# Kernel tuning notes

Measured on AMD Instinct MI355X. Metric: run time of the kernel, lower is better.

The kernel has to match this reference:

```python
import jax, jax.numpy as jnp
import numpy as np

C_Z, H, C = 128, 4, 32
L = 320
SCALE = 1.0 / np.sqrt(C)
EPS = 1e-5


def setup_inputs() -> dict:
    key = jax.random.key(0)
    ks = jax.random.split(key, 8)
    s = 0.02
    return {
        "z": jax.random.normal(ks[0], (L, L, C_Z), dtype=jnp.float32),
        "pair_mask": jnp.ones((L, L), dtype=jnp.float32),
        "res_mask": jnp.ones((L,), dtype=bool),
        "ln_gamma": jnp.ones((C_Z,), dtype=jnp.float32),
        "ln_beta": jnp.zeros((C_Z,), dtype=jnp.float32),
        "Wq": jax.random.normal(ks[1], (C_Z, H * C), dtype=jnp.float32) * s,
        "Wk": jax.random.normal(ks[2], (C_Z, H * C), dtype=jnp.float32) * s,
        "Wv": jax.random.normal(ks[3], (C_Z, H * C), dtype=jnp.float32) * s,
        "Wb": jax.random.normal(ks[4], (C_Z, H), dtype=jnp.float32) * s,
        "Wg": jax.random.normal(ks[5], (C_Z, H * C), dtype=jnp.float32) * s,
        "Wout": jax.random.normal(ks[6], (H * C, C_Z), dtype=jnp.float32) * s,
    }


def _layernorm(x, gamma, beta):
    mu = jnp.mean(x, axis=-1, keepdims=True)
    var = jnp.mean(jnp.square(x - mu), axis=-1, keepdims=True)
    return (x - mu) * jax.lax.rsqrt(var + EPS) * gamma + beta


def reference(z, pair_mask, res_mask, ln_gamma, ln_beta, Wq, Wk, Wv, Wb, Wg, Wout):
    Ldim = z.shape[0]
    z_ln = _layernorm(z, ln_gamma, ln_beta)                      # [L,L,c_z]
    Q = (z_ln @ Wq).reshape(Ldim, Ldim, H, C)                    # [i,j,h,c]
    K = (z_ln @ Wk).reshape(Ldim, Ldim, H, C)                    # [i,k,h,c]
    V = (z_ln @ Wv).reshape(Ldim, Ldim, H, C)                    # [i,k,h,c]
    B = z_ln @ Wb                                                # [j,k,h]
    G = jax.nn.sigmoid(z_ln @ Wg).reshape(Ldim, Ldim, H, C)      # [i,j,h,c]

    # logits[i,h,j,k] = <Q[i,j], K[i,k]> * scale + B[j,k,h]
    logits = jnp.einsum("ijhc,ikhc->ihjk", Q, K) * SCALE
    logits = logits + jnp.transpose(B, (2, 0, 1))[None]          # +[1,h,j,k]
    neg_inf = jnp.asarray(-jnp.inf, logits.dtype)
    logits = jnp.where(res_mask[None, None, None, :], logits, neg_inf)
    attn = jax.nn.softmax(logits, axis=-1)                       # over k

    out = jnp.einsum("ihjk,ikhc->ijhc", attn, V)                 # [i,j,h,c]
    out = (G * out).reshape(Ldim, Ldim, H * C)
    dz = out @ Wout                                              # [L,L,c_z]
    return dz * pair_mask[..., None]
```

## Files before the change

kernel.cpp:

```cpp
#include <hip/hip_runtime.h>

#define LDIM 320
#define CZ 128
#define NH 4
#define CH 32
#define SCALE_QK 0.17677669529663687f
#define LN_EPS 1e-5f

typedef __attribute__((ext_vector_type(8))) short bf16x8;
typedef __attribute__((ext_vector_type(4))) float f32x4;

__device__ __forceinline__ unsigned int pack_bf2(float a, float b) {
  unsigned int ua = __float_as_uint(a);
  unsigned int ub = __float_as_uint(b);
  unsigned int ra = (ua + 0x7fffu + ((ua >> 16) & 1u)) >> 16;
  unsigned int rb = (ub + 0x7fffu + ((ub >> 16) & 1u)) >> 16;
  return (ra & 0xffffu) | (rb << 16);
}

__device__ __forceinline__ unsigned short f2bf(float a) {
  unsigned int ua = __float_as_uint(a);
  return (unsigned short)((ua + 0x7fffu + ((ua >> 16) & 1u)) >> 16);
}

__device__ __forceinline__ float bf2f(unsigned short u) {
  return __uint_as_float(((unsigned int)u) << 16);
}

__global__ __launch_bounds__(256) void k_prep(
    const float* __restrict__ Wq, const float* __restrict__ Wk,
    const float* __restrict__ Wv, const float* __restrict__ Wb,
    const float* __restrict__ Wg, const float* __restrict__ Wout,
    unsigned short* __restrict__ Wt, unsigned short* __restrict__ Woutt)
{
  __shared__ __attribute__((aligned(16))) unsigned short buf[64 * 136];
  const int t = threadIdx.x, bid = blockIdx.x;
  const bool isOut = (bid >= 9);
  const int n0 = isOut ? (bid - 9) * 64 : bid * 64;
  const int nl = t & 63;
  const int n = n0 + nl;
#pragma unroll 8
  for (int it = 0; it < 32; ++it) {
    const int k = (t >> 6) + 4 * it;
    float v;
    if (isOut)        v = Wout[k * 128 + n];
    else if (n < 128) v = Wq[k * 128 + n];
    else if (n < 256) v = Wk[k * 128 + n - 128];
    else if (n < 384) v = Wv[k * 128 + n - 256];
    else if (n < 512) v = Wg[k * 128 + n - 384];
    else if (n < 516) v = Wb[k * 4 + n - 512];
    else              v = 0.f;
    buf[nl * 136 + k] = f2bf(v);
  }
  __syncthreads();
  unsigned short* dst = isOut ? Woutt : Wt;
#pragma unroll
  for (int it = 0; it < 4; ++it) {
    const int idx = t + 256 * it;
    const int rr = idx >> 4, ck = idx & 15;
    const uint4 d = *(const uint4*)&buf[rr * 136 + ck * 8];
    *(uint4*)(dst + (size_t)(n0 + rr) * 128 + ck * 8) = d;
  }
}

__global__ __launch_bounds__(256) void k_lnproj(
    const float* __restrict__ z, const float* __restrict__ gamma,
    const float* __restrict__ beta, const unsigned short* __restrict__ Wt,
    unsigned short* __restrict__ Qg, unsigned short* __restrict__ Kg,
    unsigned short* __restrict__ Vg, unsigned short* __restrict__ Gg,
    float* __restrict__ Bh)
{
  __shared__ __attribute__((aligned(16))) unsigned short As[128 * 136];
  const int t = threadIdx.x;
  const int m0 = blockIdx.x * 128;
  const int rlane = t & 7;

  const float* gp = gamma + rlane * 16;
  const float* bp = beta + rlane * 16;
  const float4 g0 = *(const float4*)(gp + 0);
  const float4 g1 = *(const float4*)(gp + 4);
  const float4 g2 = *(const float4*)(gp + 8);
  const float4 g3 = *(const float4*)(gp + 12);
  const float4 b0 = *(const float4*)(bp + 0);
  const float4 b1 = *(const float4*)(bp + 4);
  const float4 b2 = *(const float4*)(bp + 8);
  const float4 b3 = *(const float4*)(bp + 12);

#pragma unroll
  for (int rr = 0; rr < 4; ++rr) {
    const int row = rr * 32 + (t >> 3);
    const float* zp = z + (size_t)(m0 + row) * CZ + rlane * 16;
    const float4 x0 = *(const float4*)(zp + 0);
    const float4 x1 = *(const float4*)(zp + 4);
    const float4 x2 = *(const float4*)(zp + 8);
    const float4 x3 = *(const float4*)(zp + 12);
    float s  = x0.x + x0.y + x0.z + x0.w + x1.x + x1.y + x1.z + x1.w +
               x2.x + x2.y + x2.z + x2.w + x3.x + x3.y + x3.z + x3.w;
    float ss = x0.x*x0.x + x0.y*x0.y + x0.z*x0.z + x0.w*x0.w +
               x1.x*x1.x + x1.y*x1.y + x1.z*x1.z + x1.w*x1.w +
               x2.x*x2.x + x2.y*x2.y + x2.z*x2.z + x2.w*x2.w +
               x3.x*x3.x + x3.y*x3.y + x3.z*x3.z + x3.w*x3.w;
    s  += __shfl_xor(s, 1);  ss += __shfl_xor(ss, 1);
    s  += __shfl_xor(s, 2);  ss += __shfl_xor(ss, 2);
    s  += __shfl_xor(s, 4);  ss += __shfl_xor(ss, 4);
    const float mu  = s * (1.f / 128.f);
    const float var = ss * (1.f / 128.f) - mu * mu;
    const float rs  = rsqrtf(var + LN_EPS);
    uint4 u0, u1;
    u0.x = pack_bf2((x0.x - mu) * rs * g0.x + b0.x, (x0.y - mu) * rs * g0.y + b0.y);
    u0.y = pack_bf2((x0.z - mu) * rs * g0.z + b0.z, (x0.w - mu) * rs * g0.w + b0.w);
    u0.z = pack_bf2((x1.x - mu) * rs * g1.x + b1.x, (x1.y - mu) * rs * g1.y + b1.y);
    u0.w = pack_bf2((x1.z - mu) * rs * g1.z + b1.z, (x1.w - mu) * rs * g1.w + b1.w);
    u1.x = pack_bf2((x2.x - mu) * rs * g2.x + b2.x, (x2.y - mu) * rs * g2.y + b2.y);
    u1.y = pack_bf2((x2.z - mu) * rs * g2.z + b2.z, (x2.w - mu) * rs * g2.w + b2.w);
    u1.z = pack_bf2((x3.x - mu) * rs * g3.x + b3.x, (x3.y - mu) * rs * g3.y + b3.y);
    u1.w = pack_bf2((x3.z - mu) * rs * g3.z + b3.z, (x3.w - mu) * rs * g3.w + b3.w);
    unsigned short* dst = &As[row * 136 + rlane * 16];
    *(uint4*)(dst + 0) = u0;
    *(uint4*)(dst + 8) = u1;
  }
  __syncthreads();

  const int w = t >> 6, lane = t & 63;
  const int m16 = lane & 15, qd = lane >> 4;
  const f32x4 z4 = {0.f, 0.f, 0.f, 0.f};

  bf16x8 af[2][4];
#pragma unroll
  for (int ks = 0; ks < 4; ++ks) {
    af[0][ks] = *(const bf16x8*)&As[(w * 32 + m16) * 136 + ks * 32 + qd * 8];
    af[1][ks] = *(const bf16x8*)&As[(w * 32 + 16 + m16) * 136 + ks * 32 + qd * 8];
  }

  for (int ntile = 0; ntile < 8; ++ntile) {
    f32x4 acc[2][4];
#pragma unroll
    for (int sub = 0; sub < 2; ++sub)
#pragma unroll
      for (int nt = 0; nt < 4; ++nt) acc[sub][nt] = z4;
#pragma unroll
    for (int ks = 0; ks < 4; ++ks) {
#pragma unroll
      for (int nt = 0; nt < 4; ++nt) {
        const bf16x8 bf = *(const bf16x8*)(
            Wt + (size_t)(ntile * 64 + nt * 16 + m16) * 128 + ks * 32 + qd * 8);
        acc[0][nt] = __builtin_amdgcn_mfma_f32_16x16x32_bf16(af[0][ks], bf, acc[0][nt], 0, 0, 0);
        acc[1][nt] = __builtin_amdgcn_mfma_f32_16x16x32_bf16(af[1][ks], bf, acc[1][nt], 0, 0, 0);
      }
    }
#pragma unroll
    for (int sub = 0; sub < 2; ++sub) {
#pragma unroll
      for (int r = 0; r < 4; ++r) {
        const int p = m0 + w * 32 + sub * 16 + qd * 4 + r;
        const int a = p / 320, bb = p - a * 320;
#pragma unroll
        for (int nt = 0; nt < 4; ++nt) {
          const int n = ntile * 64 + nt * 16 + m16;
          const int off = n & 127, hh = off >> 5, cc = off & 31;
          float val = acc[sub][nt][r];
          if (ntile >= 6) val = 1.f / (1.f + __expf(-val));
          unsigned short* dst =
              (ntile < 2 ? Qg : (ntile < 4 ? Kg : (ntile < 6 ? Vg : Gg)));
          dst[((size_t)(a * 4 + hh) * 320 + bb) * 32 + cc] = f2bf(val);
        }
      }
    }
  }

  {
    f32x4 acc0 = z4, acc1 = z4;
#pragma unroll
    for (int ks = 0; ks < 4; ++ks) {
      const bf16x8 bf = *(const bf16x8*)(
          Wt + (size_t)(512 + m16) * 128 + ks * 32 + qd * 8);
      acc0 = __builtin_amdgcn_mfma_f32_16x16x32_bf16(af[0][ks], bf, acc0, 0, 0, 0);
      acc1 = __builtin_amdgcn_mfma_f32_16x16x32_bf16(af[1][ks], bf, acc1, 0, 0, 0);
    }
    if (m16 < 4) {
#pragma unroll
      for (int r = 0; r < 4; ++r) {
        const int p0 = m0 + w * 32 + qd * 4 + r;
        Bh[(size_t)m16 * 102400 + p0] = acc0[r];
        Bh[(size_t)m16 * 102400 + p0 + 16] = acc1[r];
      }
    }
  }
}

__global__ __launch_bounds__(256) void k_attn(
    const unsigned short* __restrict__ Qg, const unsigned short* __restrict__ Kg,
    const unsigned short* __restrict__ Vg, const unsigned short* __restrict__ Gg,
    const float* __restrict__ Bh, const int* __restrict__ rmask,
    unsigned short* __restrict__ Obg)
{
  __shared__ __attribute__((aligned(16))) unsigned short Vt[32 * 328];
  __shared__ __attribute__((aligned(16))) unsigned short Ps[4][16 * 168];
  const int h = blockIdx.x, i = blockIdx.y;
  const int t = threadIdx.x;
  const size_t base = (size_t)(i * NH + h) * (LDIM * CH);

  {
    const int k0 = t >> 3, c4 = (t & 7) * 4;
#pragma unroll
    for (int it = 0; it < 10; ++it) {
      const int k = k0 + 32 * it;
      const uint2 d = *(const uint2*)(Vg + base + k * 32 + c4);
      Vt[(c4 + 0) * 328 + k] = (unsigned short)(d.x & 0xffffu);
      Vt[(c4 + 1) * 328 + k] = (unsigned short)(d.x >> 16);
      Vt[(c4 + 2) * 328 + k] = (unsigned short)(d.y & 0xffffu);
      Vt[(c4 + 3) * 328 + k] = (unsigned short)(d.y >> 16);
    }
  }
  __syncthreads();

  const int w = t >> 6, lane = t & 63;
  const int m16 = lane & 15, qd = lane >> 4;
  const f32x4 z4 = {0.f, 0.f, 0.f, 0.f};

  float mkr[20];
#pragma unroll
  for (int kt = 0; kt < 20; ++kt)
    mkr[kt] = rmask[kt * 16 + m16] ? 0.f : -INFINITY;

  for (int jt = w; jt < 20; jt += 4) {
    const bf16x8 qfrag =
        *(const bf16x8*)(Qg + base + (size_t)(jt * 16 + m16) * 32 + qd * 8);

    f32x4 acc[20];
#pragma unroll
    for (int kt = 0; kt < 20; ++kt) {
      const bf16x8 kf =
          *(const bf16x8*)(Kg + base + (size_t)(kt * 16 + m16) * 32 + qd * 8);
      acc[kt] = __builtin_amdgcn_mfma_f32_16x16x32_bf16(qfrag, kf, z4, 0, 0, 0);
    }

    const float* bp = Bh + (size_t)h * 102400 +
                      (size_t)(jt * 16 + qd * 4) * 320 + m16;
    float mx[4] = {-INFINITY, -INFINITY, -INFINITY, -INFINITY};
#pragma unroll
    for (int kt = 0; kt < 20; ++kt) {
#pragma unroll
      for (int r = 0; r < 4; ++r) {
        const float b = bp[r * 320 + kt * 16];
        const float s = fmaf(acc[kt][r], SCALE_QK, b) + mkr[kt];
        acc[kt][r] = s;
        mx[r] = fmaxf(mx[r], s);
      }
    }
#pragma unroll
    for (int r = 0; r < 4; ++r) {
      mx[r] = fmaxf(mx[r], __shfl_xor(mx[r], 1));
      mx[r] = fmaxf(mx[r], __shfl_xor(mx[r], 2));
      mx[r] = fmaxf(mx[r], __shfl_xor(mx[r], 4));
      mx[r] = fmaxf(mx[r], __shfl_xor(mx[r], 8));
    }
    float l[4] = {0.f, 0.f, 0.f, 0.f};
#pragma unroll
    for (int kt = 0; kt < 20; ++kt) {
#pragma unroll
      for (int r = 0; r < 4; ++r) {
        const float p = __expf(acc[kt][r] - mx[r]);
        acc[kt][r] = p;
        l[r] += p;
      }
    }
#pragma unroll
    for (int r = 0; r < 4; ++r) {
      l[r] += __shfl_xor(l[r], 1);
      l[r] += __shfl_xor(l[r], 2);
      l[r] += __shfl_xor(l[r], 4);
      l[r] += __shfl_xor(l[r], 8);
    }
    float rl[4];
#pragma unroll
    for (int r = 0; r < 4; ++r) rl[r] = 1.f / l[r];

    f32x4 accO0 = z4, accO1 = z4;
#pragma unroll
    for (int hh = 0; hh < 2; ++hh) {
      __syncthreads();
#pragma unroll
      for (int kt2 = 0; kt2 < 10; ++kt2) {
        const int kt = hh * 10 + kt2;
#pragma unroll
        for (int r = 0; r < 4; ++r)
          Ps[w][(qd * 4 + r) * 168 + kt2 * 16 + m16] = f2bf(acc[kt][r] * rl[r]);
      }
      __syncthreads();
#pragma unroll
      for (int ks = 0; ks < 5; ++ks) {
        const bf16x8 pf = *(const bf16x8*)&Ps[w][m16 * 168 + ks * 32 + qd * 8];
        const bf16x8 v0 =
            *(const bf16x8*)&Vt[m16 * 328 + hh * 160 + ks * 32 + qd * 8];
        const bf16x8 v1 =
            *(const bf16x8*)&Vt[(16 + m16) * 328 + hh * 160 + ks * 32 + qd * 8];
        accO0 = __builtin_amdgcn_mfma_f32_16x16x32_bf16(pf, v0, accO0, 0, 0, 0);
        accO1 = __builtin_amdgcn_mfma_f32_16x16x32_bf16(pf, v1, accO1, 0, 0, 0);
      }
    }

#pragma unroll
    for (int r = 0; r < 4; ++r) {
      const int j = jt * 16 + qd * 4 + r;
      const float g0 = bf2f(Gg[base + (size_t)j * 32 + m16]);
      const float g1 = bf2f(Gg[base + (size_t)j * 32 + 16 + m16]);
      unsigned short* op = Obg + (size_t)(i * 320 + j) * 128 + h * 32;
      op[m16]      = f2bf(g0 * accO0[r]);
      op[16 + m16] = f2bf(g1 * accO1[r]);
    }
  }
}

__global__ __launch_bounds__(256) void k_out(
    const unsigned short* __restrict__ Obg, const unsigned short* __restrict__ Woutt,
    const float* __restrict__ pm, float* __restrict__ out)
{
  __shared__ __attribute__((aligned(16))) unsigned short As[128 * 136];
  __shared__ __attribute__((aligned(16))) unsigned short Bs[64 * 136];
  const int t = threadIdx.x;
  const int ntile = blockIdx.x;
  const int m0 = blockIdx.y * 128;

#pragma unroll
  for (int it = 0; it < 8; ++it) {
    const int idx = t + 256 * it;
    const int rr = idx >> 4, ck = idx & 15;
    const uint4 d = *(const uint4*)(Obg + (size_t)(m0 + rr) * 128 + ck * 8);
    *(uint4*)&As[rr * 136 + ck * 8] = d;
  }
  {
    const unsigned short* wrow = Woutt + (size_t)ntile * 64 * 128;
#pragma unroll
    for (int it = 0; it < 4; ++it) {
      const int idx = t + 256 * it;
      const int n = idx >> 4, ck = idx & 15;
      const uint4 d = *(const uint4*)(wrow + n * 128 + ck * 8);
      *(uint4*)&Bs[n * 136 + ck * 8] = d;
    }
  }
  __syncthreads();

  const int w = t >> 6, lane = t & 63;
  const int m16 = lane & 15, qd = lane >> 4;
  const f32x4 z4 = {0.f, 0.f, 0.f, 0.f};
  f32x4 acc[2][4];
#pragma unroll
  for (int sub = 0; sub < 2; ++sub)
#pragma unroll
    for (int nt = 0; nt < 4; ++nt) acc[sub][nt] = z4;

#pragma unroll
  for (int ks = 0; ks < 4; ++ks) {
    const bf16x8 af0 = *(const bf16x8*)&As[(w * 32 + m16) * 136 + qd * 8 + ks * 32];
    const bf16x8 af1 = *(const bf16x8*)&As[(w * 32 + 16 + m16) * 136 + qd * 8 + ks * 32];
#pragma unroll
    for (int nt = 0; nt < 4; ++nt) {
      const bf16x8 bf = *(const bf16x8*)&Bs[(nt * 16 + m16) * 136 + qd * 8 + ks * 32];
      acc[0][nt] = __builtin_amdgcn_mfma_f32_16x16x32_bf16(af0, bf, acc[0][nt], 0, 0, 0);
      acc[1][nt] = __builtin_amdgcn_mfma_f32_16x16x32_bf16(af1, bf, acc[1][nt], 0, 0, 0);
    }
  }

#pragma unroll
  for (int sub = 0; sub < 2; ++sub) {
#pragma unroll
    for (int r = 0; r < 4; ++r) {
      const int p = m0 + w * 32 + sub * 16 + qd * 4 + r;
      const float m = pm[p];
      float* orow = out + (size_t)p * 128 + ntile * 64;
#pragma unroll
      for (int nt = 0; nt < 4; ++nt)
        orow[nt * 16 + m16] = acc[sub][nt][r] * m;
    }
  }
}

extern "C" void kernel_launch(void* const* d_in, const int* in_sizes, int n_in,
                              void* d_out, int out_size, void* d_ws, size_t ws_size,
                              hipStream_t stream)
{
  const float* z     = (const float*)d_in[0];
  const float* pmask = (const float*)d_in[1];
  const int*   rmask = (const int*)d_in[2];
  const float* gamma = (const float*)d_in[3];
  const float* beta  = (const float*)d_in[4];
  const float* Wq    = (const float*)d_in[5];
  const float* Wk    = (const float*)d_in[6];
  const float* Wv    = (const float*)d_in[7];
  const float* Wb    = (const float*)d_in[8];
  const float* Wg    = (const float*)d_in[9];
  const float* Wout  = (const float*)d_in[10];

  const size_t P = (size_t)LDIM * LDIM;
  const size_t E = P * 128;
  char* ws = (char*)d_ws;
  unsigned short* Qg = (unsigned short*)ws;
  unsigned short* Kg = Qg + E;
  unsigned short* Vg = Kg + E;
  unsigned short* Gg = Vg + E;
  unsigned short* Obg = Gg + E;
  unsigned short* Wt = Obg + E;
  unsigned short* Woutt = Wt + 576 * 128;
  float* Bh = (float*)(Woutt + 128 * 128);

  k_prep<<<dim3(11), 256, 0, stream>>>(Wq, Wk, Wv, Wb, Wg, Wout, Wt, Woutt);
  k_lnproj<<<dim3(800), 256, 0, stream>>>(z, gamma, beta, Wt,
                                          Qg, Kg, Vg, Gg, Bh);
  k_attn<<<dim3(NH, LDIM), 256, 0, stream>>>(Qg, Kg, Vg, Gg, Bh, rmask, Obg);
  k_out<<<dim3(2, 800), 256, 0, stream>>>(Obg, Woutt, pmask, (float*)d_out);
}
```

Before: 352.0 us.

## Fold mask and log2e into bias, use exp2, drop syncs, defer softmax normalization

The residue mask and the log2(e) factor move into the bias computed in the projection kernel, so the attention kernel needs one FMA per logit and can use a native exp2 and a fast reciprocal. Softmax normalization is deferred to the output stage, where it is fused with the gate multiply, instead of being applied per probability. The block-wide __syncthreads around the per-wave P buffer are removed because each wave only touches its own slice, and s_setprio is raised around the MFMA loops. Rounding changes slightly because unnormalized probabilities are stored in bf16, and fully masked rows would still give NaN as before.

```diff
diff --git a/kernel.cpp b/kernel.cpp
--- a/kernel.cpp
+++ b/kernel.cpp
@@ -4,7 +4,8 @@
 #define CZ 128
 #define NH 4
 #define CH 32
-#define SCALE_QK 0.17677669529663687f
+#define SCALE2F (0.17677669529663687f * 1.4426950408889634f)
+#define LOG2E 1.4426950408889634f
 #define LN_EPS 1e-5f
 
 typedef __attribute__((ext_vector_type(8))) short bf16x8;
@@ -66,6 +67,7 @@
 __global__ __launch_bounds__(256) void k_lnproj(
     const float* __restrict__ z, const float* __restrict__ gamma,
     const float* __restrict__ beta, const unsigned short* __restrict__ Wt,
+    const int* __restrict__ rmask,
     unsigned short* __restrict__ Qg, unsigned short* __restrict__ Kg,
     unsigned short* __restrict__ Vg, unsigned short* __restrict__ Gg,
     float* __restrict__ Bh)
@@ -181,8 +183,11 @@
 #pragma unroll
       for (int r = 0; r < 4; ++r) {
         const int p0 = m0 + w * 32 + qd * 4 + r;
-        Bh[(size_t)m16 * 102400 + p0] = acc0[r];
-        Bh[(size_t)m16 * 102400 + p0 + 16] = acc1[r];
+        const int p1 = p0 + 16;
+        const float mk0 = rmask[p0 % 320] ? 0.f : -INFINITY;
+        const float mk1 = rmask[p1 % 320] ? 0.f : -INFINITY;
+        Bh[(size_t)m16 * 102400 + p0] = acc0[r] * LOG2E + mk0;
+        Bh[(size_t)m16 * 102400 + p1] = acc1[r] * LOG2E + mk1;
       }
     }
   }
@@ -191,8 +196,7 @@
 __global__ __launch_bounds__(256) void k_attn(
     const unsigned short* __restrict__ Qg, const unsigned short* __restrict__ Kg,
     const unsigned short* __restrict__ Vg, const unsigned short* __restrict__ Gg,
-    const float* __restrict__ Bh, const int* __restrict__ rmask,
-    unsigned short* __restrict__ Obg)
+    const float* __restrict__ Bh, unsigned short* __restrict__ Obg)
 {
   __shared__ __attribute__((aligned(16))) unsigned short Vt[32 * 328];
   __shared__ __attribute__((aligned(16))) unsigned short Ps[4][16 * 168];
@@ -218,22 +222,19 @@
   const int m16 = lane & 15, qd = lane >> 4;
   const f32x4 z4 = {0.f, 0.f, 0.f, 0.f};
 
-  float mkr[20];
-#pragma unroll
-  for (int kt = 0; kt < 20; ++kt)
-    mkr[kt] = rmask[kt * 16 + m16] ? 0.f : -INFINITY;
-
   for (int jt = w; jt < 20; jt += 4) {
     const bf16x8 qfrag =
         *(const bf16x8*)(Qg + base + (size_t)(jt * 16 + m16) * 32 + qd * 8);
 
     f32x4 acc[20];
+    __builtin_amdgcn_s_setprio(1);
 #pragma unroll
     for (int kt = 0; kt < 20; ++kt) {
       const bf16x8 kf =
           *(const bf16x8*)(Kg + base + (size_t)(kt * 16 + m16) * 32 + qd * 8);
       acc[kt] = __builtin_amdgcn_mfma_f32_16x16x32_bf16(qfrag, kf, z4, 0, 0, 0);
     }
+    __builtin_amdgcn_s_setprio(0);
 
     const float* bp = Bh + (size_t)h * 102400 +
                       (size_t)(jt * 16 + qd * 4) * 320 + m16;
@@ -242,8 +243,7 @@
     for (int kt = 0; kt < 20; ++kt) {
 #pragma unroll
       for (int r = 0; r < 4; ++r) {
-        const float b = bp[r * 320 + kt * 16];
-        const float s = fmaf(acc[kt][r], SCALE_QK, b) + mkr[kt];
+        const float s = fmaf(acc[kt][r], SCALE2F, bp[r * 320 + kt * 16]);
         acc[kt][r] = s;
         mx[r] = fmaxf(mx[r], s);
       }
@@ -260,7 +260,7 @@
     for (int kt = 0; kt < 20; ++kt) {
 #pragma unroll
       for (int r = 0; r < 4; ++r) {
-        const float p = __expf(acc[kt][r] - mx[r]);
+        const float p = __builtin_amdgcn_exp2f(acc[kt][r] - mx[r]);
         acc[kt][r] = p;
         l[r] += p;
       }
@@ -274,20 +274,19 @@
     }
     float rl[4];
 #pragma unroll
-    for (int r = 0; r < 4; ++r) rl[r] = 1.f / l[r];
+    for (int r = 0; r < 4; ++r) rl[r] = __builtin_amdgcn_rcpf(l[r]);
 
     f32x4 accO0 = z4, accO1 = z4;
 #pragma unroll
     for (int hh = 0; hh < 2; ++hh) {
-      __syncthreads();
 #pragma unroll
       for (int kt2 = 0; kt2 < 10; ++kt2) {
         const int kt = hh * 10 + kt2;
 #pragma unroll
         for (int r = 0; r < 4; ++r)
-          Ps[w][(qd * 4 + r) * 168 + kt2 * 16 + m16] = f2bf(acc[kt][r] * rl[r]);
-      }
-      __syncthreads();
+          Ps[w][(qd * 4 + r) * 168 + kt2 * 16 + m16] = f2bf(acc[kt][r]);
+      }
+      __builtin_amdgcn_s_setprio(1);
 #pragma unroll
       for (int ks = 0; ks < 5; ++ks) {
         const bf16x8 pf = *(const bf16x8*)&Ps[w][m16 * 168 + ks * 32 + qd * 8];
@@ -298,6 +297,7 @@
         accO0 = __builtin_amdgcn_mfma_f32_16x16x32_bf16(pf, v0, accO0, 0, 0, 0);
         accO1 = __builtin_amdgcn_mfma_f32_16x16x32_bf16(pf, v1, accO1, 0, 0, 0);
       }
+      __builtin_amdgcn_s_setprio(0);
     }
 
 #pragma unroll
@@ -306,8 +306,8 @@
       const float g0 = bf2f(Gg[base + (size_t)j * 32 + m16]);
       const float g1 = bf2f(Gg[base + (size_t)j * 32 + 16 + m16]);
       unsigned short* op = Obg + (size_t)(i * 320 + j) * 128 + h * 32;
-      op[m16]      = f2bf(g0 * accO0[r]);
-      op[16 + m16] = f2bf(g1 * accO1[r]);
+      op[m16]      = f2bf(g0 * rl[r] * accO0[r]);
+      op[16 + m16] = f2bf(g1 * rl[r] * accO1[r]);
     }
   }
 }
@@ -405,8 +405,8 @@
   float* Bh = (float*)(Woutt + 128 * 128);
 
   k_prep<<<dim3(11), 256, 0, stream>>>(Wq, Wk, Wv, Wb, Wg, Wout, Wt, Woutt);
-  k_lnproj<<<dim3(800), 256, 0, stream>>>(z, gamma, beta, Wt,
+  k_lnproj<<<dim3(800), 256, 0, stream>>>(z, gamma, beta, Wt, rmask,
                                           Qg, Kg, Vg, Gg, Bh);
-  k_attn<<<dim3(NH, LDIM), 256, 0, stream>>>(Qg, Kg, Vg, Gg, Bh, rmask, Obg);
+  k_attn<<<dim3(NH, LDIM), 256, 0, stream>>>(Qg, Kg, Vg, Gg, Bh, Obg);
   k_out<<<dim3(2, 800), 256, 0, stream>>>(Obg, Woutt, pmask, (float*)d_out);
 }
```

New measurement: 348.5 us. About the same (-1.0%).
